# Optimization experiments

Hardware: AMD Instinct MI355X
Metric: run time of the kernel (lower is better)

The kernel has to match this reference:

```python
import jax, jax.numpy as jnp
import numpy as np

N = 2048        # num_nodes
E = 32768       # num input edges (avg degree 16)
F = 8           # edge feature dim
E_MAX = 1_048_576  # static padding for output edge count (expected ~525K two-hop + 32K orig)


def setup_inputs() -> dict:
    key = jax.random.key(0)
    k1, k2, k3 = jax.random.split(key, 3)
    src = jax.random.randint(k1, (E,), 0, N, dtype=jnp.int32)
    dst = jax.random.randint(k2, (E,), 0, N, dtype=jnp.int32)
    edge_index = jnp.stack([src, dst])                     # [2, E]
    edge_attr = jax.random.normal(k3, (E, F), dtype=jnp.float32)
    return {"num_nodes": N, "edge_index": edge_index, "edge_attr": edge_attr}


def reference(num_nodes, edge_index, edge_attr):
    n = num_nodes
    f = edge_attr.shape[1]
    src, dst = edge_index[0], edge_index[1]

    # to_torch_coo_tensor: adjacency with ones. Dense stand-in for SpGEMM.
    A = jnp.zeros((n, n), jnp.float32).at[src, dst].set(1.0)   # presence (input assumed coalesced)
    A2 = A @ A                                                  # path counts; structure of adj @ adj

    # remove_self_loops on the two-hop edges
    mask2 = (A2 > 0) & (~jnp.eye(n, dtype=bool))

    # original edge mask
    orig = jnp.zeros((n, n), dtype=bool).at[src, dst].set(True)

    # coalesce: union of edge sets, sorted lexicographically by (row, col).
    combined = orig | mask2

    # coalesce reduce='sum': duplicates of original edges sum their attrs;
    # two-hop-only edges contribute zeros (edge_attr2 = new_zeros).
    attr_dense = jnp.zeros((n, n, f), edge_attr.dtype).at[src, dst].add(edge_attr)

    # row-major nonzero == lexicographic (row, col) sort; static size via padding.
    rows, cols = jnp.nonzero(combined, size=E_MAX, fill_value=0)
    count = combined.sum()
    valid = jnp.arange(E_MAX) < count

    out_edge_index = jnp.stack([
        jnp.where(valid, rows, -1),
        jnp.where(valid, cols, -1),
    ]).astype(jnp.int32)                                        # [2, E_MAX], -1 padded
    out_attr = attr_dense[rows, cols] * valid[:, None]          # [E_MAX, F], zero padded
    return out_edge_index, out_attr
```

## Files before the change

kernel.cpp:

```cpp
#include <hip/hip_runtime.h>

#define N_NODES 2048
#define WORDS   64
#define E_MAX_OUT 1048576
#define FDIM    8


__global__ void k_init(float* __restrict__ out, unsigned* __restrict__ a_bits) {
    int tid = blockIdx.x * blockDim.x + threadIdx.x;
    int nthreads = gridDim.x * blockDim.x;
    const int TOTAL4 = (2 * E_MAX_OUT + FDIM * E_MAX_OUT) / 4;
    const int NEG4   = (2 * E_MAX_OUT) / 4;
    float4* o4 = (float4*)out;
    for (int p = tid; p < TOTAL4; p += nthreads) {
        float v = (p < NEG4) ? -1.0f : 0.0f;
        o4[p] = make_float4(v, v, v, v);
    }
    for (int p = tid; p < N_NODES * WORDS; p += nthreads) a_bits[p] = 0u;
}

__global__ void k_build(const int* __restrict__ ei, int E, unsigned* __restrict__ a_bits) {
    int e = blockIdx.x * blockDim.x + threadIdx.x;
    if (e >= E) return;
    int s = ei[e];
    int d = ei[E + e];
    atomicOr(&a_bits[s * WORDS + (d >> 5)], 1u << (d & 31));
}

__global__ void __launch_bounds__(256) k_twohop(const unsigned* __restrict__ a_bits,
                                                unsigned* __restrict__ c_bits,
                                                int* __restrict__ rel_off,
                                                int* __restrict__ row_cnt) {
    int lane = threadIdx.x & 63;
    int wv   = threadIdx.x >> 6;
    int i    = blockIdx.x * 4 + wv;
    __shared__ int nbr[4][256];
    __shared__ int ncnt_sh[4];

    unsigned r = a_bits[i * WORDS + lane];
    int pc = __popc(r);
    int incl = pc;
    for (int off = 1; off < 64; off <<= 1) {
        int v = __shfl_up(incl, off, 64);
        if (lane >= off) incl += v;
    }
    int base = incl - pc;
    unsigned bits = r;
    int wb = lane << 5;
    while (bits) {
        int b = __ffs(bits) - 1;
        bits &= bits - 1;
        nbr[wv][base++] = wb + b;
    }
    if (lane == 63) ncnt_sh[wv] = incl;
    __syncthreads();

    int nc = ncnt_sh[wv];
    const int* nb = nbr[wv];
    unsigned acc = 0u;
    int j = 0;
    for (; j + 4 <= nc; j += 4) {
        unsigned x0 = a_bits[nb[j]     * WORDS + lane];
        unsigned x1 = a_bits[nb[j + 1] * WORDS + lane];
        unsigned x2 = a_bits[nb[j + 2] * WORDS + lane];
        unsigned x3 = a_bits[nb[j + 3] * WORDS + lane];
        acc |= (x0 | x1) | (x2 | x3);
    }
    for (; j < nc; ++j) acc |= a_bits[nb[j] * WORDS + lane];

    if (lane == (i >> 5)) acc &= ~(1u << (i & 31));
    acc |= r;
    c_bits[i * WORDS + lane] = acc;

    int cnt = __popc(acc);
    int incl2 = cnt;
    for (int off = 1; off < 64; off <<= 1) {
        int v = __shfl_up(incl2, off, 64);
        if (lane >= off) incl2 += v;
    }
    rel_off[i * WORDS + lane] = incl2 - cnt;
    if (lane == 63) row_cnt[i] = incl2;
}

__global__ void __launch_bounds__(64) k_scan(const int* __restrict__ row_cnt,
                                             int* __restrict__ row_off) {
    int t = threadIdx.x;
    int base = t * 32;
    int c[32];
    int s = 0;
    #pragma unroll
    for (int q = 0; q < 32; ++q) { c[q] = row_cnt[base + q]; s += c[q]; }
    int incl = s;
    for (int off = 1; off < 64; off <<= 1) {
        int v = __shfl_up(incl, off, 64);
        if (t >= off) incl += v;
    }
    int run = incl - s;
    #pragma unroll
    for (int q = 0; q < 32; ++q) { row_off[base + q] = run; run += c[q]; }
    if (t == 63) row_off[N_NODES] = incl;
}

__global__ void __launch_bounds__(128) k_emit_attr(const unsigned* __restrict__ c_bits,
                                                   const int* __restrict__ rel_off,
                                                   const int* __restrict__ row_off,
                                                   const int* __restrict__ ei,
                                                   const float* __restrict__ attr, int E,
                                                   float* __restrict__ out) {
    int i    = blockIdx.x;
    int lane = threadIdx.x & 63;
    int wave = threadIdx.x >> 6;

    if (wave == 0) {
        unsigned c = c_bits[i * WORDS + lane];
        int p = row_off[i] + rel_off[i * WORDS + lane];
        float fi = (float)i;
        int wb = lane << 5;
        unsigned bits = c;
        while (bits) {
            int b = __ffs(bits) - 1;
            bits &= bits - 1;
            if (p < E_MAX_OUT) {
                out[p]             = fi;
                out[E_MAX_OUT + p] = (float)(wb + b);
            }
            ++p;
        }
    } else {
        float* oattr = out + 2 * E_MAX_OUT;
        for (int e = i * 16 + (lane >> 2); e < E; e += N_NODES * 16) {
            int s = ei[e];
            int d = ei[E + e];
            int dw = d >> 5;
            unsigned cw = c_bits[s * WORDS + dw];
            int p = row_off[s] + rel_off[s * WORDS + dw]
                  + __popc(cw & ((1u << (d & 31)) - 1u));
            if (p < E_MAX_OUT) {
                int q = lane & 3;
                atomicAdd(&oattr[p * FDIM + 2 * q],     attr[e * FDIM + 2 * q]);
                atomicAdd(&oattr[p * FDIM + 2 * q + 1], attr[e * FDIM + 2 * q + 1]);
            }
        }
    }
}

extern "C" void kernel_launch(void* const* d_in, const int* in_sizes, int n_in,
                              void* d_out, int out_size, void* d_ws, size_t ws_size,
                              hipStream_t stream) {
    const int*   ei   = (const int*)d_in[1];
    const float* attr = (const float*)d_in[2];
    int E = in_sizes[1] / 2;

    float* out = (float*)d_out;
    unsigned char* ws = (unsigned char*)d_ws;
    unsigned* a_bits  = (unsigned*)(ws);
    unsigned* c_bits  = (unsigned*)(ws + 512 * 1024);
    int*      rel_off = (int*)(ws + 1024 * 1024);
    int*      row_cnt = (int*)(ws + 1536 * 1024);
    int*      row_off = (int*)(ws + 1536 * 1024 + 16 * 1024);

    k_init     <<<2048, 256, 0, stream>>>(out, a_bits);
    k_build    <<<(E + 255) / 256, 256, 0, stream>>>(ei, E, a_bits);
    k_twohop   <<<N_NODES / 4, 256, 0, stream>>>(a_bits, c_bits, rel_off, row_cnt);
    k_scan     <<<1, 64, 0, stream>>>(row_cnt, row_off);
    k_emit_attr<<<N_NODES, 128, 0, stream>>>(c_bits, rel_off, row_off, ei, attr, E, out);
}
```

Before: 30.01 us.

## Fuse row scan and padding fill into emit; bucket edges per source row

Removes the single-block scan kernel: each emit block now reduces row_cnt itself to get its row offset and the total count. The -1 padding of the index outputs is written by the emit blocks over only the tail past count, so init now zeroes just the attribute region. The build kernel also puts edges into per-source lists (capped at 64 per row), so each emit block handles only its own row's edges and skips the per-edge source lookup. This saves a launch and redundant index writes, but every block repeats a 2048-element reduction. Any row with more than 64 out-edges would silently lose attributes, and the bounds checks on output positions are gone.

Result: slower. 32.27 us (+7.5%).

```diff
diff --git a/kernel.cpp b/kernel.cpp
--- a/kernel.cpp
+++ b/kernel.cpp
@@ -4,27 +4,30 @@
 #define WORDS   64
 #define E_MAX_OUT 1048576
 #define FDIM    8
+#define EL_CAP  64
 
 
-__global__ void k_init(float* __restrict__ out, unsigned* __restrict__ a_bits) {
+__global__ void k_init(float* __restrict__ out_attr, unsigned* __restrict__ a_bits,
+                       int* __restrict__ ecnt) {
     int tid = blockIdx.x * blockDim.x + threadIdx.x;
-    int nthreads = gridDim.x * blockDim.x;
-    const int TOTAL4 = (2 * E_MAX_OUT + FDIM * E_MAX_OUT) / 4;
-    const int NEG4   = (2 * E_MAX_OUT) / 4;
-    float4* o4 = (float4*)out;
-    for (int p = tid; p < TOTAL4; p += nthreads) {
-        float v = (p < NEG4) ? -1.0f : 0.0f;
-        o4[p] = make_float4(v, v, v, v);
-    }
-    for (int p = tid; p < N_NODES * WORDS; p += nthreads) a_bits[p] = 0u;
+    int nth = gridDim.x * blockDim.x;
+    const int A4 = FDIM * E_MAX_OUT / 4;
+    float4* o4 = (float4*)out_attr;
+    for (int p = tid; p < A4; p += nth) o4[p] = make_float4(0.f, 0.f, 0.f, 0.f);
+    uint4* a4 = (uint4*)a_bits;
+    for (int p = tid; p < N_NODES * WORDS / 4; p += nth) a4[p] = make_uint4(0u, 0u, 0u, 0u);
+    for (int p = tid; p < N_NODES; p += nth) ecnt[p] = 0;
 }
 
-__global__ void k_build(const int* __restrict__ ei, int E, unsigned* __restrict__ a_bits) {
+__global__ void k_build(const int* __restrict__ ei, int E, unsigned* __restrict__ a_bits,
+                        int* __restrict__ ecnt, int* __restrict__ elist) {
     int e = blockIdx.x * blockDim.x + threadIdx.x;
     if (e >= E) return;
     int s = ei[e];
     int d = ei[E + e];
     atomicOr(&a_bits[s * WORDS + (d >> 5)], 1u << (d & 31));
+    int slot = atomicAdd(&ecnt[s], 1);
+    if (slot < EL_CAP) elist[s * EL_CAP + slot] = e;
 }
 
 __global__ void __launch_bounds__(256) k_twohop(const unsigned* __restrict__ a_bits,
@@ -82,65 +85,71 @@
     if (lane == 63) row_cnt[i] = incl2;
 }
 
-__global__ void __launch_bounds__(64) k_scan(const int* __restrict__ row_cnt,
-                                             int* __restrict__ row_off) {
-    int t = threadIdx.x;
-    int base = t * 32;
-    int c[32];
-    int s = 0;
-    #pragma unroll
-    for (int q = 0; q < 32; ++q) { c[q] = row_cnt[base + q]; s += c[q]; }
-    int incl = s;
-    for (int off = 1; off < 64; off <<= 1) {
-        int v = __shfl_up(incl, off, 64);
-        if (t >= off) incl += v;
-    }
-    int run = incl - s;
-    #pragma unroll
-    for (int q = 0; q < 32; ++q) { row_off[base + q] = run; run += c[q]; }
-    if (t == 63) row_off[N_NODES] = incl;
-}
-
 __global__ void __launch_bounds__(128) k_emit_attr(const unsigned* __restrict__ c_bits,
                                                    const int* __restrict__ rel_off,
-                                                   const int* __restrict__ row_off,
+                                                   const int* __restrict__ row_cnt,
                                                    const int* __restrict__ ei,
                                                    const float* __restrict__ attr, int E,
+                                                   const int* __restrict__ ecnt,
+                                                   const int* __restrict__ elist,
                                                    float* __restrict__ out) {
     int i    = blockIdx.x;
-    int lane = threadIdx.x & 63;
-    int wave = threadIdx.x >> 6;
+    int t    = threadIdx.x;
+    int lane = t & 63;
+    int wave = t >> 6;
+    __shared__ int sh_lt[2], sh_all[2];
+
+    int p_lt = 0, p_all = 0;
+    #pragma unroll
+    for (int q = 0; q < N_NODES / 128; ++q) {
+        int idx = t * (N_NODES / 128) + q;
+        int v = row_cnt[idx];
+        p_all += v;
+        if (idx < i) p_lt += v;
+    }
+    for (int off = 32; off; off >>= 1) {
+        p_lt  += __shfl_down(p_lt,  off, 64);
+        p_all += __shfl_down(p_all, off, 64);
+    }
+    if (lane == 0) { sh_lt[wave] = p_lt; sh_all[wave] = p_all; }
+    __syncthreads();
+    int row_off_i = sh_lt[0] + sh_lt[1];
+    int count     = sh_all[0] + sh_all[1];
 
     if (wave == 0) {
         unsigned c = c_bits[i * WORDS + lane];
-        int p = row_off[i] + rel_off[i * WORDS + lane];
+        int p = row_off_i + rel_off[i * WORDS + lane];
         float fi = (float)i;
         int wb = lane << 5;
-        unsigned bits = c;
-        while (bits) {
-            int b = __ffs(bits) - 1;
-            bits &= bits - 1;
-            if (p < E_MAX_OUT) {
-                out[p]             = fi;
-                out[E_MAX_OUT + p] = (float)(wb + b);
-            }
+        while (c) {
+            int b = __ffs(c) - 1;
+            c &= c - 1;
+            out[p]             = fi;
+            out[E_MAX_OUT + p] = (float)(wb + b);
             ++p;
         }
     } else {
         float* oattr = out + 2 * E_MAX_OUT;
-        for (int e = i * 16 + (lane >> 2); e < E; e += N_NODES * 16) {
-            int s = ei[e];
+        int ne = ecnt[i];
+        int q  = lane & 3;
+        for (int slot = lane >> 2; slot < ne; slot += 16) {
+            int e = elist[i * EL_CAP + slot];
             int d = ei[E + e];
             int dw = d >> 5;
-            unsigned cw = c_bits[s * WORDS + dw];
-            int p = row_off[s] + rel_off[s * WORDS + dw]
+            unsigned cw = c_bits[i * WORDS + dw];
+            int p = row_off_i + rel_off[i * WORDS + dw]
                   + __popc(cw & ((1u << (d & 31)) - 1u));
-            if (p < E_MAX_OUT) {
-                int q = lane & 3;
-                atomicAdd(&oattr[p * FDIM + 2 * q],     attr[e * FDIM + 2 * q]);
-                atomicAdd(&oattr[p * FDIM + 2 * q + 1], attr[e * FDIM + 2 * q + 1]);
-            }
+            atomicAdd(&oattr[p * FDIM + 2 * q],     attr[e * FDIM + 2 * q]);
+            atomicAdd(&oattr[p * FDIM + 2 * q + 1], attr[e * FDIM + 2 * q + 1]);
         }
+    }
+
+    long long P = (long long)(E_MAX_OUT - count);
+    int s0 = count + (int)(P * i / N_NODES);
+    int s1 = count + (int)(P * (i + 1) / N_NODES);
+    for (int p = s0 + t; p < s1; p += 128) {
+        out[p]             = -1.0f;
+        out[E_MAX_OUT + p] = -1.0f;
     }
 }
 
@@ -157,11 +166,12 @@
     unsigned* c_bits  = (unsigned*)(ws + 512 * 1024);
     int*      rel_off = (int*)(ws + 1024 * 1024);
     int*      row_cnt = (int*)(ws + 1536 * 1024);
-    int*      row_off = (int*)(ws + 1536 * 1024 + 16 * 1024);
+    int*      ecnt    = (int*)(ws + 1544 * 1024);
+    int*      elist   = (int*)(ws + 1552 * 1024);
 
-    k_init     <<<2048, 256, 0, stream>>>(out, a_bits);
-    k_build    <<<(E + 255) / 256, 256, 0, stream>>>(ei, E, a_bits);
+    k_init     <<<2048, 256, 0, stream>>>(out + 2 * E_MAX_OUT, a_bits, ecnt);
+    k_build    <<<(E + 255) / 256, 256, 0, stream>>>(ei, E, a_bits, ecnt, elist);
     k_twohop   <<<N_NODES / 4, 256, 0, stream>>>(a_bits, c_bits, rel_off, row_cnt);
-    k_scan     <<<1, 64, 0, stream>>>(row_cnt, row_off);
-    k_emit_attr<<<N_NODES, 128, 0, stream>>>(c_bits, rel_off, row_off, ei, attr, E, out);
+    k_emit_attr<<<N_NODES, 128, 0, stream>>>(c_bits, rel_off, row_cnt, ei, attr, E,
+                                             ecnt, elist, out);
 }
```
